# Performance work log

Hardware: AMD Instinct MI355X
Metric: run time of the kernel (lower is better)

The kernel has to match this reference:

```python
import jax, jax.numpy as jnp
import numpy as np

N, E, IN_C, HID_C, OUT_C = 50000, 800000, 64, 64, 8
NEG_SLOPE = 0.2


def setup_inputs() -> dict:
    key = jax.random.key(0)
    ks = jax.random.split(key, 12)
    return {
        "x": jax.random.normal(ks[0], (N, IN_C), dtype=jnp.float32),
        "edge_index": jax.random.randint(ks[1], (2, E), 0, N, dtype=jnp.int64),
        "edge_value": jax.random.uniform(ks[2], (E,), dtype=jnp.float32),
        "W1": jax.random.normal(ks[3], (IN_C, HID_C), dtype=jnp.float32) * 0.1,
        "a1_src": jax.random.normal(ks[4], (HID_C,), dtype=jnp.float32) * 0.1,
        "a1_dst": jax.random.normal(ks[5], (HID_C,), dtype=jnp.float32) * 0.1,
        "b1": jnp.zeros((HID_C,), dtype=jnp.float32),
        "W2": jax.random.normal(ks[6], (HID_C, OUT_C), dtype=jnp.float32) * 0.1,
        "a2_src": jax.random.normal(ks[7], (OUT_C,), dtype=jnp.float32) * 0.1,
        "a2_dst": jax.random.normal(ks[8], (OUT_C,), dtype=jnp.float32) * 0.1,
        "b2": jnp.zeros((OUT_C,), dtype=jnp.float32),
    }


def _rgat_conv(x, src, dst, edge_value, W, a_src, a_dst, b, n_nodes):
    # Linear transform: [N, out_c]
    h = x @ W
    # Per-node attention halves, gathered per edge -> per-edge logit
    e_src = h @ a_src  # [N]
    e_dst = h @ a_dst  # [N]
    logits = jax.nn.leaky_relu(e_src[src] + e_dst[dst], negative_slope=NEG_SLOPE)  # [E]
    # Segment softmax over destination neighborhoods (numerically stable)
    m = jax.ops.segment_max(logits, dst, num_segments=n_nodes)  # [N]
    ex = jnp.exp(logits - m[dst])
    denom = jax.ops.segment_sum(ex, dst, num_segments=n_nodes)  # [N]
    alpha = ex / (denom[dst] + 1e-16)  # [E]
    # Edge-weighted messages, scatter-aggregate to destinations
    msg = (alpha * edge_value)[:, None] * h[src]  # [E, out_c]
    out = jax.ops.segment_sum(msg, dst, num_segments=n_nodes)  # [N, out_c]
    return out + b


def reference(x, edge_index, edge_value, W1, a1_src, a1_dst, b1, W2, a2_src, a2_dst, b2):
    src, dst = edge_index[0], edge_index[1]
    n = x.shape[0]
    hid = _rgat_conv(x, src, dst, edge_value, W1, a1_src, a1_dst, b1, n)
    hid = jax.nn.relu(hid)
    out = _rgat_conv(hid, src, dst, edge_value, W2, a2_src, a2_dst, b2, n)
    return jax.nn.log_softmax(out, axis=1)
```

## Files before the change

kernel.cpp:

```cpp
#include <hip/hip_runtime.h>
#include <hip/hip_fp16.h>
#include <math.h>


#define CHUNK 4096
#define NBKT  256
#define CAP   6144

typedef unsigned long long ull;
typedef float v2f __attribute__((ext_vector_type(2)));

struct PartSmem {
    int lhist[NBKT], lbase[NBKT], lcur[NBKT], gbase[NBKT];
    ull buf[CHUNK];
};
struct GemmSmem {
    float4 Wl[64 * 16];
    float  Xt[64 * 64];
};
union FusedSmem { PartSmem p; GemmSmem g; };


__global__ void __launch_bounds__(256) part_gemm_kernel(
    const int* __restrict__ src, const int* __restrict__ dst,
    const float* __restrict__ ev, int* __restrict__ bcnt,
    ull* __restrict__ ped, int E, int nchunks,
    const float* __restrict__ x, const float* __restrict__ W,
    const float* __restrict__ a_src, const float* __restrict__ a_dst,
    unsigned* __restrict__ h, float* __restrict__ es, float* __restrict__ ed,
    int N)
{
    __shared__ FusedSmem sm;
    const int t = threadIdx.x;

    if (blockIdx.x < nchunks) {
        int e0 = blockIdx.x * CHUNK;
        int cnt = min(CHUNK, E - e0);
        sm.p.lhist[t] = 0;
        __syncthreads();
        for (int i = t; i < cnt; i += 256)
            atomicAdd(&sm.p.lhist[dst[e0 + i] >> 8], 1);
        __syncthreads();
        int myc = sm.p.lhist[t];
        sm.p.lbase[t] = myc;
        __syncthreads();
        for (int o = 1; o < 256; o <<= 1) {
            int add = (t >= o) ? sm.p.lbase[t - o] : 0;
            __syncthreads();
            sm.p.lbase[t] += add;
            __syncthreads();
        }
        int excl = sm.p.lbase[t] - myc;
        sm.p.gbase[t] = myc ? atomicAdd(&bcnt[t], myc) : 0;
        __syncthreads();
        sm.p.lbase[t] = excl;
        sm.p.lcur[t] = excl;
        __syncthreads();
        for (int i = t; i < cnt; i += 256) {
            int e = e0 + i;
            int d = dst[e];
            int b = d >> 8;
            unsigned p = (unsigned)src[e] | ((unsigned)(d & 255) << 16)
                       | ((unsigned)b << 24);
            ull q = (ull)p | ((ull)__float_as_uint(ev[e]) << 32);
            int r = atomicAdd(&sm.p.lcur[b], 1);
            sm.p.buf[r] = q;
        }
        __syncthreads();
        for (int i = t; i < cnt; i += 256) {
            ull q = sm.p.buf[i];
            int b = (int)((q >> 24) & 255);
            ped[(size_t)b * CAP + sm.p.gbase[b] + i - sm.p.lbase[b]] = q;
        }
        return;
    }

    const int n0 = (blockIdx.x - nchunks) * 64;

    #pragma unroll
    for (int i = 0; i < 4; ++i)
        sm.g.Wl[t + i * 256] = ((const float4*)W)[t + i * 256];

    #pragma unroll
    for (int i = 0; i < 4; ++i) {
        int f   = t + i * 256;
        int row = f >> 4, kq = f & 15;
        int grow = n0 + row;
        float4 v = make_float4(0.f, 0.f, 0.f, 0.f);
        if (grow < N) v = ((const float4*)x)[(size_t)grow * 16 + kq];
        int rs = row ^ ((kq & 3) << 2);
        sm.g.Xt[(kq * 4 + 0) * 64 + rs] = v.x;
        sm.g.Xt[(kq * 4 + 1) * 64 + rs] = v.y;
        sm.g.Xt[(kq * 4 + 2) * 64 + rs] = v.z;
        sm.g.Xt[(kq * 4 + 3) * 64 + rs] = v.w;
    }

    const int tx = t & 15;
    const int ty = t >> 4;
    const float4 asv = ((const float4*)a_src)[tx];
    const float4 adv = ((const float4*)a_dst)[tx];
    __syncthreads();

    float4 acc0 = make_float4(0.f,0.f,0.f,0.f);
    float4 acc1 = make_float4(0.f,0.f,0.f,0.f);
    float4 acc2 = make_float4(0.f,0.f,0.f,0.f);
    float4 acc3 = make_float4(0.f,0.f,0.f,0.f);

    #pragma unroll 8
    for (int k = 0; k < 64; ++k) {
        int swz = (k >> 2) & 3;
        const float4 xr = *(const float4*)&sm.g.Xt[k * 64 + ((ty ^ swz) << 2)];
        const float4 wv = sm.g.Wl[k * 16 + tx];
        acc0.x += xr.x * wv.x; acc0.y += xr.x * wv.y;
        acc0.z += xr.x * wv.z; acc0.w += xr.x * wv.w;
        acc1.x += xr.y * wv.x; acc1.y += xr.y * wv.y;
        acc1.z += xr.y * wv.z; acc1.w += xr.y * wv.w;
        acc2.x += xr.z * wv.x; acc2.y += xr.z * wv.y;
        acc2.z += xr.z * wv.z; acc2.w += xr.z * wv.w;
        acc3.x += xr.w * wv.x; acc3.y += xr.w * wv.y;
        acc3.z += xr.w * wv.z; acc3.w += xr.w * wv.w;
    }

    float4 accs[4] = {acc0, acc1, acc2, acc3};
    #pragma unroll
    for (int r = 0; r < 4; ++r) {
        int grow = n0 + ty * 4 + r;
        float4 a = accs[r];
        if (grow < N) {
            int lo = __builtin_amdgcn_cvt_pk_fp8_f32(a.x, a.y, 0, false);
            int pk = __builtin_amdgcn_cvt_pk_fp8_f32(a.z, a.w, lo, true);
            h[(size_t)grow * 16 + tx] = (unsigned)pk;
        }
        float ps = a.x * asv.x + a.y * asv.y + a.z * asv.z + a.w * asv.w;
        float pd = a.x * adv.x + a.y * adv.y + a.z * adv.z + a.w * adv.w;
        #pragma unroll
        for (int o = 8; o > 0; o >>= 1) {
            ps += __shfl_xor(ps, o);
            pd += __shfl_xor(pd, o);
        }
        if (tx == 0 && grow < N) { es[grow] = ps; ed[grow] = pd; }
    }
}


__global__ void __launch_bounds__(1024) csr2_kernel(
    const ull* __restrict__ ped, const int* __restrict__ bcnt,
    int* __restrict__ off, int* __restrict__ deg,
    ull* __restrict__ csre, int N)
{
    __shared__ int cl[256], sc[256], cur[256];
    int b = blockIdx.x, t = threadIdx.x;
    const int cnt = min(bcnt[b], CAP);
    const size_t base = (size_t)b * CAP;
    if (t < 256) cl[t] = 0;
    __syncthreads();
    for (int i = t; i < cnt; i += 1024)
        atomicAdd(&cl[(int)((ped[base + i] >> 16) & 255)], 1);
    __syncthreads();
    int myc = (t < 256) ? cl[t] : 0;
    if (t < 256) sc[t] = myc;
    __syncthreads();
    for (int o = 1; o < 256; o <<= 1) {
        int add = (t >= o && t < 256) ? sc[t - o] : 0;
        __syncthreads();
        if (t < 256) sc[t] += add;
        __syncthreads();
    }
    if (t < 256) {
        int excl = sc[t] - myc;
        int node = b * 256 + t;
        if (node < N) { off[node] = (int)base + excl; deg[node] = myc; }
        cur[t] = excl;
    }
    __syncthreads();
    for (int i = t; i < cnt; i += 1024) {
        ull q = ped[base + i];
        int dloc = (int)((q >> 16) & 255);
        int pos = (int)base + atomicAdd(&cur[dloc], 1);
        csre[pos] = (q & 0xFFFFFFFF00000000ull) | (q & 0xFFFFull);
    }
}


__global__ void __launch_bounds__(256) agg64_fused_kernel(
    const int* __restrict__ off, const int* __restrict__ deg,
    const ull* __restrict__ csre,
    const float* __restrict__ es, const float* __restrict__ ed,
    const unsigned* __restrict__ h, const float* __restrict__ b1,
    const float* __restrict__ W2, const float* __restrict__ a2s,
    const float* __restrict__ a2d, float* __restrict__ h2,
    float* __restrict__ es2, float* __restrict__ ed2, int N)
{
    __shared__ float W2s[64 * 8];
    const int t = threadIdx.x;
    if (t < 128) ((float4*)W2s)[t] = ((const float4*)W2)[t];

    const int wid = t >> 6, lane = t & 63;
    const int grp = lane >> 2;
    const int sl  = lane & 3;
    const int gbase = grp << 2;
    const int n = (blockIdx.x * 4 + wid) * 16 + grp;
    __syncthreads();
    if (n >= N) return;

    const int   beg = off[n];
    const int   dg  = deg[n];
    const float edn = ed[n];

    const float4 b1v0 = *(const float4*)&b1[sl * 16];
    const float4 b1v1 = *(const float4*)&b1[sl * 16 + 4];
    const float4 b1v2 = *(const float4*)&b1[sl * 16 + 8];
    const float4 b1v3 = *(const float4*)&b1[sl * 16 + 12];

    float acc[16];
    #pragma unroll
    for (int k = 0; k < 16; ++k) acc[k] = 0.f;
    float den = 0.f;

    for (int j0 = 0; j0 < dg; j0 += 4) {
        const int jj  = j0 + sl;
        const ull rec = csre[beg + min(jj, dg - 1)];
        const int sv  = (int)(rec & 0xFFFFull);
        const float evv = __uint_as_float((unsigned)(rec >> 32));
        float z = es[sv] + edn;
        float l = z > 0.f ? z : 0.2f * z;
        float q = (jj < dg) ? __expf(l) : 0.f;
        den += q;
        const float w = q * evv;
        #pragma unroll
        for (int ts = 0; ts < 4; ++ts) {
            const int   svt = __shfl(sv, gbase + ts);
            const float wt  = __shfl(w,  gbase + ts);
            const uint4 u = *(const uint4*)&h[(size_t)svt * 16 + sl * 4];
            v2f fa = __builtin_amdgcn_cvt_pk_f32_fp8((int)u.x, false);
            v2f fb = __builtin_amdgcn_cvt_pk_f32_fp8((int)u.x, true);
            v2f fc = __builtin_amdgcn_cvt_pk_f32_fp8((int)u.y, false);
            v2f fd = __builtin_amdgcn_cvt_pk_f32_fp8((int)u.y, true);
            v2f fe = __builtin_amdgcn_cvt_pk_f32_fp8((int)u.z, false);
            v2f ff = __builtin_amdgcn_cvt_pk_f32_fp8((int)u.z, true);
            v2f fg = __builtin_amdgcn_cvt_pk_f32_fp8((int)u.w, false);
            v2f fh = __builtin_amdgcn_cvt_pk_f32_fp8((int)u.w, true);
            acc[0]  += wt * fa.x; acc[1]  += wt * fa.y;
            acc[2]  += wt * fb.x; acc[3]  += wt * fb.y;
            acc[4]  += wt * fc.x; acc[5]  += wt * fc.y;
            acc[6]  += wt * fd.x; acc[7]  += wt * fd.y;
            acc[8]  += wt * fe.x; acc[9]  += wt * fe.y;
            acc[10] += wt * ff.x; acc[11] += wt * ff.y;
            acc[12] += wt * fg.x; acc[13] += wt * fg.y;
            acc[14] += wt * fh.x; acc[15] += wt * fh.y;
        }
    }

    den += __shfl_xor(den, 1);
    den += __shfl_xor(den, 2);
    const float inv = 1.f / (den + 1e-16f);

    float hid[16];
    hid[0]  = fmaxf(acc[0]  * inv + b1v0.x, 0.f);
    hid[1]  = fmaxf(acc[1]  * inv + b1v0.y, 0.f);
    hid[2]  = fmaxf(acc[2]  * inv + b1v0.z, 0.f);
    hid[3]  = fmaxf(acc[3]  * inv + b1v0.w, 0.f);
    hid[4]  = fmaxf(acc[4]  * inv + b1v1.x, 0.f);
    hid[5]  = fmaxf(acc[5]  * inv + b1v1.y, 0.f);
    hid[6]  = fmaxf(acc[6]  * inv + b1v1.z, 0.f);
    hid[7]  = fmaxf(acc[7]  * inv + b1v1.w, 0.f);
    hid[8]  = fmaxf(acc[8]  * inv + b1v2.x, 0.f);
    hid[9]  = fmaxf(acc[9]  * inv + b1v2.y, 0.f);
    hid[10] = fmaxf(acc[10] * inv + b1v2.z, 0.f);
    hid[11] = fmaxf(acc[11] * inv + b1v2.w, 0.f);
    hid[12] = fmaxf(acc[12] * inv + b1v3.x, 0.f);
    hid[13] = fmaxf(acc[13] * inv + b1v3.y, 0.f);
    hid[14] = fmaxf(acc[14] * inv + b1v3.z, 0.f);
    hid[15] = fmaxf(acc[15] * inv + b1v3.w, 0.f);

    float p[8];
    #pragma unroll
    for (int o = 0; o < 8; ++o) p[o] = 0.f;
    #pragma unroll
    for (int k = 0; k < 16; ++k) {
        const float4 wA = *(const float4*)&W2s[(sl * 16 + k) * 8];
        const float4 wB = *(const float4*)&W2s[(sl * 16 + k) * 8 + 4];
        p[0] += hid[k] * wA.x; p[1] += hid[k] * wA.y;
        p[2] += hid[k] * wA.z; p[3] += hid[k] * wA.w;
        p[4] += hid[k] * wB.x; p[5] += hid[k] * wB.y;
        p[6] += hid[k] * wB.z; p[7] += hid[k] * wB.w;
    }
    float s4[4];
    {
        const bool hi = (sl & 1);
        #pragma unroll
        for (int k = 0; k < 4; ++k) {
            float keep = hi ? p[k + 4] : p[k];
            float send = hi ? p[k]     : p[k + 4];
            s4[k] = keep + __shfl_xor(send, 1);
        }
    }
    float s2[2];
    {
        const bool hi = (sl & 2);
        #pragma unroll
        for (int k = 0; k < 2; ++k) {
            float keep = hi ? s4[k + 2] : s4[k];
            float send = hi ? s4[k]     : s4[k + 2];
            s2[k] = keep + __shfl_xor(send, 2);
        }
    }
    const int oo = 4 * (sl & 1) + 2 * ((sl >> 1) & 1);

    float tsv = s2[0] * a2s[oo] + s2[1] * a2s[oo + 1];
    float tdv = s2[0] * a2d[oo] + s2[1] * a2d[oo + 1];
    tsv += __shfl_xor(tsv, 1); tdv += __shfl_xor(tdv, 1);
    tsv += __shfl_xor(tsv, 2); tdv += __shfl_xor(tdv, 2);

    *(float2*)&h2[(size_t)n * 8 + oo] = make_float2(s2[0], s2[1]);
    if (sl == 0) { es2[n] = tsv; ed2[n] = tdv; }
}


__global__ void __launch_bounds__(256) agg8_lsm_kernel(
    const int* __restrict__ off, const int* __restrict__ deg,
    const ull* __restrict__ csre,
    const float* __restrict__ es, const float* __restrict__ ed,
    const float* __restrict__ h2, const float* __restrict__ b,
    float* __restrict__ out, int N)
{
    const int t = threadIdx.x;
    const int wid = t >> 6, lane = t & 63;
    const int grp = lane >> 2;
    const int sl  = lane & 3;
    const int gbase = grp << 2;
    const int n = (blockIdx.x * 4 + wid) * 16 + grp;
    if (n >= N) return;

    const int   beg = off[n];
    const int   dg  = deg[n];
    const float edn = ed[n];
    const float bc0 = b[2 * sl], bc1 = b[2 * sl + 1];

    float a0 = 0.f, a1 = 0.f, den = 0.f;

    for (int j0 = 0; j0 < dg; j0 += 4) {
        const int jj  = j0 + sl;
        const ull rec = csre[beg + min(jj, dg - 1)];
        const int sv  = (int)(rec & 0xFFFFull);
        const float evv = __uint_as_float((unsigned)(rec >> 32));
        float z = es[sv] + edn;
        float l = z > 0.f ? z : 0.2f * z;
        float q = (jj < dg) ? __expf(l) : 0.f;
        den += q;
        const float w = q * evv;
        #pragma unroll
        for (int ts = 0; ts < 4; ++ts) {
            const int   svt = __shfl(sv, gbase + ts);
            const float wt  = __shfl(w,  gbase + ts);
            const float2 f = *(const float2*)&h2[(size_t)svt * 8 + 2 * sl];
            a0 += wt * f.x;
            a1 += wt * f.y;
        }
    }

    den += __shfl_xor(den, 1);
    den += __shfl_xor(den, 2);
    const float inv = 1.f / (den + 1e-16f);
    float v0 = a0 * inv + bc0;
    float v1 = a1 * inv + bc1;

    float vm = fmaxf(v0, v1);
    vm = fmaxf(vm, __shfl_xor(vm, 1));
    vm = fmaxf(vm, __shfl_xor(vm, 2));
    float s = __expf(v0 - vm) + __expf(v1 - vm);
    s += __shfl_xor(s, 1);
    s += __shfl_xor(s, 2);
    float lse = vm + logf(s);
    *(float2*)&out[(size_t)n * 8 + 2 * sl] = make_float2(v0 - lse, v1 - lse);
}


extern "C" void kernel_launch(void* const* d_in, const int* in_sizes, int n_in,
                              void* d_out, int out_size, void* d_ws, size_t ws_size,
                              hipStream_t stream)
{
    const float* x   = (const float*)d_in[0];
    const int*   ei  = (const int*)d_in[1];
    const float* ev  = (const float*)d_in[2];
    const float* W1  = (const float*)d_in[3];
    const float* a1s = (const float*)d_in[4];
    const float* a1d = (const float*)d_in[5];
    const float* b1  = (const float*)d_in[6];
    const float* W2  = (const float*)d_in[7];
    const float* a2s = (const float*)d_in[8];
    const float* a2d = (const float*)d_in[9];
    const float* b2  = (const float*)d_in[10];
    float* out = (float*)d_out;

    const int N = in_sizes[0] / 64;
    const int E = in_sizes[2];
    const int* srcp = ei;
    const int* dstp = ei + E;
    const int nchunks = (E + CHUNK - 1) / CHUNK;
    const int ngemm   = (N + 63) / 64;
    const int nbuck = (N + 255) / 256;

    ull*   ped  = (ull*)d_ws;
    ull*   csre = ped + (size_t)NBKT * CAP;
    int*   bcnt = (int*)(csre + (size_t)NBKT * CAP);
    int*   off  = bcnt + NBKT;
    int*   deg  = off + N;
    float* es1  = (float*)(deg + N);
    float* ed1  = es1 + N;
    float* es2  = ed1 + N;
    float* ed2  = es2 + N;
    unsigned* h1 = (unsigned*)(ed2 + N);
    float* h2   = (float*)(h1 + (size_t)N * 16);

    hipMemsetAsync(bcnt, 0, NBKT * sizeof(int), stream);

    part_gemm_kernel<<<nchunks + ngemm, 256, 0, stream>>>(
        srcp, dstp, ev, bcnt, ped, E, nchunks,
        x, W1, a1s, a1d, h1, es1, ed1, N);

    csr2_kernel<<<nbuck, 1024, 0, stream>>>(ped, bcnt, off, deg, csre, N);

    agg64_fused_kernel<<<(N + 63) / 64, 256, 0, stream>>>(
        off, deg, csre, es1, ed1, h1, b1, W2, a2s, a2d, h2, es2, ed2, N);

    agg8_lsm_kernel<<<(N + 63) / 64, 256, 0, stream>>>(
        off, deg, csre, es2, ed2, h2, b2, out, N);
}
```

Baseline: 140.4 us.

## Merge four kernels into one cooperative persistent kernel with grid syncs

Replaces the partition/GEMM, CSR build, layer-1 aggregation and layer-2 aggregation launches with one cooperative kernel. Blocks stride over the work items of each phase and meet at grid.sync() barriers between phases. The goal is to remove per-launch overhead and the gaps between kernels. In exchange, occupancy is capped to the co-resident grid, the CSR phase now runs with 256 threads per bucket instead of 1024, and grid-wide barriers cost time of their own.

Measured after the change: 356.7 us. +154.1%, slower.

```diff
diff --git a/kernel.cpp b/kernel.cpp
--- a/kernel.cpp
+++ b/kernel.cpp
@@ -1,6 +1,8 @@
 #include <hip/hip_runtime.h>
-#include <hip/hip_fp16.h>
+#include <hip/hip_cooperative_groups.h>
 #include <math.h>
+
+namespace cg = cooperative_groups;
 
 
 #define CHUNK 4096
@@ -20,26 +22,148 @@
 };
 union FusedSmem { PartSmem p; GemmSmem g; };
 
-
-__global__ void __launch_bounds__(256) part_gemm_kernel(
+__global__ void __launch_bounds__(256, 4) mega_kernel(
     const int* __restrict__ src, const int* __restrict__ dst,
     const float* __restrict__ ev, int* __restrict__ bcnt,
     ull* __restrict__ ped, int E, int nchunks,
-    const float* __restrict__ x, const float* __restrict__ W,
-    const float* __restrict__ a_src, const float* __restrict__ a_dst,
-    unsigned* __restrict__ h, float* __restrict__ es, float* __restrict__ ed,
-    int N)
+    const float* __restrict__ x, const float* __restrict__ W1,
+    const float* __restrict__ a1s, const float* __restrict__ a1d,
+    unsigned* __restrict__ h1, float* __restrict__ es1, float* __restrict__ ed1,
+    int* __restrict__ off, int* __restrict__ deg, ull* __restrict__ csre,
+    const float* __restrict__ b1, const float* __restrict__ W2,
+    const float* __restrict__ a2s, const float* __restrict__ a2d,
+    float* __restrict__ h2, float* __restrict__ es2, float* __restrict__ ed2,
+    const float* __restrict__ b2, float* __restrict__ out, int N)
 {
+    cg::grid_group grid = cg::this_grid();
     __shared__ FusedSmem sm;
-    const int t = threadIdx.x;
-
-    if (blockIdx.x < nchunks) {
-        int e0 = blockIdx.x * CHUNK;
-        int cnt = min(CHUNK, E - e0);
+    __shared__ float W2s[64 * 8];
+
+    const int t  = threadIdx.x;
+    const int nb = gridDim.x;
+    const int ngemm = (N + 63) / 64;
+    const int nbuck = (N + 255) / 256;
+    const int nt    = (N + 63) / 64;
+
+    for (int w = blockIdx.x; w < nchunks + ngemm; w += nb) {
+        if (w < nchunks) {
+            int e0 = w * CHUNK;
+            int cnt = min(CHUNK, E - e0);
+            sm.p.lhist[t] = 0;
+            __syncthreads();
+            for (int i = t; i < cnt; i += 256)
+                atomicAdd(&sm.p.lhist[dst[e0 + i] >> 8], 1);
+            __syncthreads();
+            int myc = sm.p.lhist[t];
+            sm.p.lbase[t] = myc;
+            __syncthreads();
+            for (int o = 1; o < 256; o <<= 1) {
+                int add = (t >= o) ? sm.p.lbase[t - o] : 0;
+                __syncthreads();
+                sm.p.lbase[t] += add;
+                __syncthreads();
+            }
+            int excl = sm.p.lbase[t] - myc;
+            sm.p.gbase[t] = myc ? atomicAdd(&bcnt[t], myc) : 0;
+            __syncthreads();
+            sm.p.lbase[t] = excl;
+            sm.p.lcur[t] = excl;
+            __syncthreads();
+            for (int i = t; i < cnt; i += 256) {
+                int e = e0 + i;
+                int d = dst[e];
+                int b = d >> 8;
+                unsigned p = (unsigned)src[e] | ((unsigned)(d & 255) << 16)
+                           | ((unsigned)b << 24);
+                ull q = (ull)p | ((ull)__float_as_uint(ev[e]) << 32);
+                int r = atomicAdd(&sm.p.lcur[b], 1);
+                sm.p.buf[r] = q;
+            }
+            __syncthreads();
+            for (int i = t; i < cnt; i += 256) {
+                ull q = sm.p.buf[i];
+                int b = (int)((q >> 24) & 255);
+                ped[(size_t)b * CAP + sm.p.gbase[b] + i - sm.p.lbase[b]] = q;
+            }
+        } else {
+            const int n0 = (w - nchunks) * 64;
+
+            #pragma unroll
+            for (int i = 0; i < 4; ++i)
+                sm.g.Wl[t + i * 256] = ((const float4*)W1)[t + i * 256];
+
+            #pragma unroll
+            for (int i = 0; i < 4; ++i) {
+                int f   = t + i * 256;
+                int row = f >> 4, kq = f & 15;
+                int grow = n0 + row;
+                float4 v = make_float4(0.f, 0.f, 0.f, 0.f);
+                if (grow < N) v = ((const float4*)x)[(size_t)grow * 16 + kq];
+                int rs = row ^ ((kq & 3) << 2);
+                sm.g.Xt[(kq * 4 + 0) * 64 + rs] = v.x;
+                sm.g.Xt[(kq * 4 + 1) * 64 + rs] = v.y;
+                sm.g.Xt[(kq * 4 + 2) * 64 + rs] = v.z;
+                sm.g.Xt[(kq * 4 + 3) * 64 + rs] = v.w;
+            }
+
+            const int tx = t & 15;
+            const int ty = t >> 4;
+            const float4 asv = ((const float4*)a1s)[tx];
+            const float4 adv = ((const float4*)a1d)[tx];
+            __syncthreads();
+
+            float4 acc0 = make_float4(0.f,0.f,0.f,0.f);
+            float4 acc1 = make_float4(0.f,0.f,0.f,0.f);
+            float4 acc2 = make_float4(0.f,0.f,0.f,0.f);
+            float4 acc3 = make_float4(0.f,0.f,0.f,0.f);
+
+            #pragma unroll 8
+            for (int k = 0; k < 64; ++k) {
+                int swz = (k >> 2) & 3;
+                const float4 xr = *(const float4*)&sm.g.Xt[k * 64 + ((ty ^ swz) << 2)];
+                const float4 wv = sm.g.Wl[k * 16 + tx];
+                acc0.x += xr.x * wv.x; acc0.y += xr.x * wv.y;
+                acc0.z += xr.x * wv.z; acc0.w += xr.x * wv.w;
+                acc1.x += xr.y * wv.x; acc1.y += xr.y * wv.y;
+                acc1.z += xr.y * wv.z; acc1.w += xr.y * wv.w;
+                acc2.x += xr.z * wv.x; acc2.y += xr.z * wv.y;
+                acc2.z += xr.z * wv.z; acc2.w += xr.z * wv.w;
+                acc3.x += xr.w * wv.x; acc3.y += xr.w * wv.y;
+                acc3.z += xr.w * wv.z; acc3.w += xr.w * wv.w;
+            }
+
+            float4 accs[4] = {acc0, acc1, acc2, acc3};
+            #pragma unroll
+            for (int r = 0; r < 4; ++r) {
+                int grow = n0 + ty * 4 + r;
+                float4 a = accs[r];
+                if (grow < N) {
+                    int lo = __builtin_amdgcn_cvt_pk_fp8_f32(a.x, a.y, 0, false);
+                    int pk = __builtin_amdgcn_cvt_pk_fp8_f32(a.z, a.w, lo, true);
+                    h1[(size_t)grow * 16 + tx] = (unsigned)pk;
+                }
+                float ps = a.x * asv.x + a.y * asv.y + a.z * asv.z + a.w * asv.w;
+                float pd = a.x * adv.x + a.y * adv.y + a.z * adv.z + a.w * adv.w;
+                #pragma unroll
+                for (int o = 8; o > 0; o >>= 1) {
+                    ps += __shfl_xor(ps, o);
+                    pd += __shfl_xor(pd, o);
+                }
+                if (tx == 0 && grow < N) { es1[grow] = ps; ed1[grow] = pd; }
+            }
+        }
+        __syncthreads();
+    }
+
+    grid.sync();
+
+    for (int b = blockIdx.x; b < nbuck; b += nb) {
+        const int cnt = min(bcnt[b], CAP);
+        const size_t base = (size_t)b * CAP;
         sm.p.lhist[t] = 0;
         __syncthreads();
         for (int i = t; i < cnt; i += 256)
-            atomicAdd(&sm.p.lhist[dst[e0 + i] >> 8], 1);
+            atomicAdd(&sm.p.lhist[(int)((ped[base + i] >> 16) & 255)], 1);
         __syncthreads();
         int myc = sm.p.lhist[t];
         sm.p.lbase[t] = myc;
@@ -51,328 +175,192 @@
             __syncthreads();
         }
         int excl = sm.p.lbase[t] - myc;
-        sm.p.gbase[t] = myc ? atomicAdd(&bcnt[t], myc) : 0;
-        __syncthreads();
-        sm.p.lbase[t] = excl;
-        sm.p.lcur[t] = excl;
-        __syncthreads();
-        for (int i = t; i < cnt; i += 256) {
-            int e = e0 + i;
-            int d = dst[e];
-            int b = d >> 8;
-            unsigned p = (unsigned)src[e] | ((unsigned)(d & 255) << 16)
-                       | ((unsigned)b << 24);
-            ull q = (ull)p | ((ull)__float_as_uint(ev[e]) << 32);
-            int r = atomicAdd(&sm.p.lcur[b], 1);
-            sm.p.buf[r] = q;
-        }
-        __syncthreads();
-        for (int i = t; i < cnt; i += 256) {
-            ull q = sm.p.buf[i];
-            int b = (int)((q >> 24) & 255);
-            ped[(size_t)b * CAP + sm.p.gbase[b] + i - sm.p.lbase[b]] = q;
-        }
-        return;
-    }
-
-    const int n0 = (blockIdx.x - nchunks) * 64;
-
-    #pragma unroll
-    for (int i = 0; i < 4; ++i)
-        sm.g.Wl[t + i * 256] = ((const float4*)W)[t + i * 256];
-
-    #pragma unroll
-    for (int i = 0; i < 4; ++i) {
-        int f   = t + i * 256;
-        int row = f >> 4, kq = f & 15;
-        int grow = n0 + row;
-        float4 v = make_float4(0.f, 0.f, 0.f, 0.f);
-        if (grow < N) v = ((const float4*)x)[(size_t)grow * 16 + kq];
-        int rs = row ^ ((kq & 3) << 2);
-        sm.g.Xt[(kq * 4 + 0) * 64 + rs] = v.x;
-        sm.g.Xt[(kq * 4 + 1) * 64 + rs] = v.y;
-        sm.g.Xt[(kq * 4 + 2) * 64 + rs] = v.z;
-        sm.g.Xt[(kq * 4 + 3) * 64 + rs] = v.w;
-    }
-
-    const int tx = t & 15;
-    const int ty = t >> 4;
-    const float4 asv = ((const float4*)a_src)[tx];
-    const float4 adv = ((const float4*)a_dst)[tx];
-    __syncthreads();
-
-    float4 acc0 = make_float4(0.f,0.f,0.f,0.f);
-    float4 acc1 = make_float4(0.f,0.f,0.f,0.f);
-    float4 acc2 = make_float4(0.f,0.f,0.f,0.f);
-    float4 acc3 = make_float4(0.f,0.f,0.f,0.f);
-
-    #pragma unroll 8
-    for (int k = 0; k < 64; ++k) {
-        int swz = (k >> 2) & 3;
-        const float4 xr = *(const float4*)&sm.g.Xt[k * 64 + ((ty ^ swz) << 2)];
-        const float4 wv = sm.g.Wl[k * 16 + tx];
-        acc0.x += xr.x * wv.x; acc0.y += xr.x * wv.y;
-        acc0.z += xr.x * wv.z; acc0.w += xr.x * wv.w;
-        acc1.x += xr.y * wv.x; acc1.y += xr.y * wv.y;
-        acc1.z += xr.y * wv.z; acc1.w += xr.y * wv.w;
-        acc2.x += xr.z * wv.x; acc2.y += xr.z * wv.y;
-        acc2.z += xr.z * wv.z; acc2.w += xr.z * wv.w;
-        acc3.x += xr.w * wv.x; acc3.y += xr.w * wv.y;
-        acc3.z += xr.w * wv.z; acc3.w += xr.w * wv.w;
-    }
-
-    float4 accs[4] = {acc0, acc1, acc2, acc3};
-    #pragma unroll
-    for (int r = 0; r < 4; ++r) {
-        int grow = n0 + ty * 4 + r;
-        float4 a = accs[r];
-        if (grow < N) {
-            int lo = __builtin_amdgcn_cvt_pk_fp8_f32(a.x, a.y, 0, false);
-            int pk = __builtin_amdgcn_cvt_pk_fp8_f32(a.z, a.w, lo, true);
-            h[(size_t)grow * 16 + tx] = (unsigned)pk;
-        }
-        float ps = a.x * asv.x + a.y * asv.y + a.z * asv.z + a.w * asv.w;
-        float pd = a.x * adv.x + a.y * adv.y + a.z * adv.z + a.w * adv.w;
-        #pragma unroll
-        for (int o = 8; o > 0; o >>= 1) {
-            ps += __shfl_xor(ps, o);
-            pd += __shfl_xor(pd, o);
-        }
-        if (tx == 0 && grow < N) { es[grow] = ps; ed[grow] = pd; }
-    }
-}
-
-
-__global__ void __launch_bounds__(1024) csr2_kernel(
-    const ull* __restrict__ ped, const int* __restrict__ bcnt,
-    int* __restrict__ off, int* __restrict__ deg,
-    ull* __restrict__ csre, int N)
-{
-    __shared__ int cl[256], sc[256], cur[256];
-    int b = blockIdx.x, t = threadIdx.x;
-    const int cnt = min(bcnt[b], CAP);
-    const size_t base = (size_t)b * CAP;
-    if (t < 256) cl[t] = 0;
-    __syncthreads();
-    for (int i = t; i < cnt; i += 1024)
-        atomicAdd(&cl[(int)((ped[base + i] >> 16) & 255)], 1);
-    __syncthreads();
-    int myc = (t < 256) ? cl[t] : 0;
-    if (t < 256) sc[t] = myc;
-    __syncthreads();
-    for (int o = 1; o < 256; o <<= 1) {
-        int add = (t >= o && t < 256) ? sc[t - o] : 0;
-        __syncthreads();
-        if (t < 256) sc[t] += add;
-        __syncthreads();
-    }
-    if (t < 256) {
-        int excl = sc[t] - myc;
         int node = b * 256 + t;
         if (node < N) { off[node] = (int)base + excl; deg[node] = myc; }
-        cur[t] = excl;
+        sm.p.lcur[t] = excl;
+        __syncthreads();
+        for (int i = t; i < cnt; i += 256) {
+            ull q = ped[base + i];
+            int dloc = (int)((q >> 16) & 255);
+            int pos = (int)base + atomicAdd(&sm.p.lcur[dloc], 1);
+            csre[pos] = (q & 0xFFFFFFFF00000000ull) | (q & 0xFFFFull);
+        }
+        __syncthreads();
     }
+
+    grid.sync();
+
+    if (t < 128) ((float4*)W2s)[t] = ((const float4*)W2)[t];
     __syncthreads();
-    for (int i = t; i < cnt; i += 1024) {
-        ull q = ped[base + i];
-        int dloc = (int)((q >> 16) & 255);
-        int pos = (int)base + atomicAdd(&cur[dloc], 1);
-        csre[pos] = (q & 0xFFFFFFFF00000000ull) | (q & 0xFFFFull);
-    }
-}
-
-
-__global__ void __launch_bounds__(256) agg64_fused_kernel(
-    const int* __restrict__ off, const int* __restrict__ deg,
-    const ull* __restrict__ csre,
-    const float* __restrict__ es, const float* __restrict__ ed,
-    const unsigned* __restrict__ h, const float* __restrict__ b1,
-    const float* __restrict__ W2, const float* __restrict__ a2s,
-    const float* __restrict__ a2d, float* __restrict__ h2,
-    float* __restrict__ es2, float* __restrict__ ed2, int N)
-{
-    __shared__ float W2s[64 * 8];
-    const int t = threadIdx.x;
-    if (t < 128) ((float4*)W2s)[t] = ((const float4*)W2)[t];
 
     const int wid = t >> 6, lane = t & 63;
-    const int grp = lane >> 2;
-    const int sl  = lane & 3;
-    const int gbase = grp << 2;
-    const int n = (blockIdx.x * 4 + wid) * 16 + grp;
-    __syncthreads();
-    if (n >= N) return;
-
-    const int   beg = off[n];
-    const int   dg  = deg[n];
-    const float edn = ed[n];
-
-    const float4 b1v0 = *(const float4*)&b1[sl * 16];
-    const float4 b1v1 = *(const float4*)&b1[sl * 16 + 4];
-    const float4 b1v2 = *(const float4*)&b1[sl * 16 + 8];
-    const float4 b1v3 = *(const float4*)&b1[sl * 16 + 12];
-
-    float acc[16];
-    #pragma unroll
-    for (int k = 0; k < 16; ++k) acc[k] = 0.f;
-    float den = 0.f;
-
-    for (int j0 = 0; j0 < dg; j0 += 4) {
-        const int jj  = j0 + sl;
-        const ull rec = csre[beg + min(jj, dg - 1)];
-        const int sv  = (int)(rec & 0xFFFFull);
-        const float evv = __uint_as_float((unsigned)(rec >> 32));
-        float z = es[sv] + edn;
-        float l = z > 0.f ? z : 0.2f * z;
-        float q = (jj < dg) ? __expf(l) : 0.f;
-        den += q;
-        const float w = q * evv;
-        #pragma unroll
-        for (int ts = 0; ts < 4; ++ts) {
-            const int   svt = __shfl(sv, gbase + ts);
-            const float wt  = __shfl(w,  gbase + ts);
-            const uint4 u = *(const uint4*)&h[(size_t)svt * 16 + sl * 4];
-            v2f fa = __builtin_amdgcn_cvt_pk_f32_fp8((int)u.x, false);
-            v2f fb = __builtin_amdgcn_cvt_pk_f32_fp8((int)u.x, true);
-            v2f fc = __builtin_amdgcn_cvt_pk_f32_fp8((int)u.y, false);
-            v2f fd = __builtin_amdgcn_cvt_pk_f32_fp8((int)u.y, true);
-            v2f fe = __builtin_amdgcn_cvt_pk_f32_fp8((int)u.z, false);
-            v2f ff = __builtin_amdgcn_cvt_pk_f32_fp8((int)u.z, true);
-            v2f fg = __builtin_amdgcn_cvt_pk_f32_fp8((int)u.w, false);
-            v2f fh = __builtin_amdgcn_cvt_pk_f32_fp8((int)u.w, true);
-            acc[0]  += wt * fa.x; acc[1]  += wt * fa.y;
-            acc[2]  += wt * fb.x; acc[3]  += wt * fb.y;
-            acc[4]  += wt * fc.x; acc[5]  += wt * fc.y;
-            acc[6]  += wt * fd.x; acc[7]  += wt * fd.y;
-            acc[8]  += wt * fe.x; acc[9]  += wt * fe.y;
-            acc[10] += wt * ff.x; acc[11] += wt * ff.y;
-            acc[12] += wt * fg.x; acc[13] += wt * fg.y;
-            acc[14] += wt * fh.x; acc[15] += wt * fh.y;
+    const int grp = lane >> 2, sl = lane & 3, gbase = grp << 2;
+
+    for (int tile = blockIdx.x; tile < nt; tile += nb) {
+        const int n = (tile * 4 + wid) * 16 + grp;
+        if (n < N) {
+            const int   beg = off[n];
+            const int   dg  = deg[n];
+            const float edn = ed1[n];
+
+            const float4 b1v0 = *(const float4*)&b1[sl * 16];
+            const float4 b1v1 = *(const float4*)&b1[sl * 16 + 4];
+            const float4 b1v2 = *(const float4*)&b1[sl * 16 + 8];
+            const float4 b1v3 = *(const float4*)&b1[sl * 16 + 12];
+
+            float acc[16];
+            #pragma unroll
+            for (int k = 0; k < 16; ++k) acc[k] = 0.f;
+            float den = 0.f;
+
+            for (int j0 = 0; j0 < dg; j0 += 4) {
+                const int jj  = j0 + sl;
+                const ull rec = csre[beg + min(jj, dg - 1)];
+                const int sv  = (int)(rec & 0xFFFFull);
+                const float evv = __uint_as_float((unsigned)(rec >> 32));
+                float z = es1[sv] + edn;
+                float l = z > 0.f ? z : 0.2f * z;
+                float q = (jj < dg) ? __expf(l) : 0.f;
+                den += q;
+                const float w = q * evv;
+                #pragma unroll
+                for (int ts = 0; ts < 4; ++ts) {
+                    const int   svt = __shfl(sv, gbase + ts);
+                    const float wt  = __shfl(w,  gbase + ts);
+                    const uint4 u = *(const uint4*)&h1[(size_t)svt * 16 + sl * 4];
+                    v2f fa = __builtin_amdgcn_cvt_pk_f32_fp8((int)u.x, false);
+                    v2f fb = __builtin_amdgcn_cvt_pk_f32_fp8((int)u.x, true);
+                    v2f fc = __builtin_amdgcn_cvt_pk_f32_fp8((int)u.y, false);
+                    v2f fd = __builtin_amdgcn_cvt_pk_f32_fp8((int)u.y, true);
+                    v2f fe = __builtin_amdgcn_cvt_pk_f32_fp8((int)u.z, false);
+                    v2f ff = __builtin_amdgcn_cvt_pk_f32_fp8((int)u.z, true);
+                    v2f fg = __builtin_amdgcn_cvt_pk_f32_fp8((int)u.w, false);
+                    v2f fh = __builtin_amdgcn_cvt_pk_f32_fp8((int)u.w, true);
+                    acc[0]  += wt * fa.x; acc[1]  += wt * fa.y;
+                    acc[2]  += wt * fb.x; acc[3]  += wt * fb.y;
+                    acc[4]  += wt * fc.x; acc[5]  += wt * fc.y;
+                    acc[6]  += wt * fd.x; acc[7]  += wt * fd.y;
+                    acc[8]  += wt * fe.x; acc[9]  += wt * fe.y;
+                    acc[10] += wt * ff.x; acc[11] += wt * ff.y;
+                    acc[12] += wt * fg.x; acc[13] += wt * fg.y;
+                    acc[14] += wt * fh.x; acc[15] += wt * fh.y;
+                }
+            }
+
+            den += __shfl_xor(den, 1);
+            den += __shfl_xor(den, 2);
+            const float inv = 1.f / (den + 1e-16f);
+
+            float hid[16];
+            hid[0]  = fmaxf(acc[0]  * inv + b1v0.x, 0.f);
+            hid[1]  = fmaxf(acc[1]  * inv + b1v0.y, 0.f);
+            hid[2]  = fmaxf(acc[2]  * inv + b1v0.z, 0.f);
+            hid[3]  = fmaxf(acc[3]  * inv + b1v0.w, 0.f);
+            hid[4]  = fmaxf(acc[4]  * inv + b1v1.x, 0.f);
+            hid[5]  = fmaxf(acc[5]  * inv + b1v1.y, 0.f);
+            hid[6]  = fmaxf(acc[6]  * inv + b1v1.z, 0.f);
+            hid[7]  = fmaxf(acc[7]  * inv + b1v1.w, 0.f);
+            hid[8]  = fmaxf(acc[8]  * inv + b1v2.x, 0.f);
+            hid[9]  = fmaxf(acc[9]  * inv + b1v2.y, 0.f);
+            hid[10] = fmaxf(acc[10] * inv + b1v2.z, 0.f);
+            hid[11] = fmaxf(acc[11] * inv + b1v2.w, 0.f);
+            hid[12] = fmaxf(acc[12] * inv + b1v3.x, 0.f);
+            hid[13] = fmaxf(acc[13] * inv + b1v3.y, 0.f);
+            hid[14] = fmaxf(acc[14] * inv + b1v3.z, 0.f);
+            hid[15] = fmaxf(acc[15] * inv + b1v3.w, 0.f);
+
+            float p[8];
+            #pragma unroll
+            for (int o = 0; o < 8; ++o) p[o] = 0.f;
+            #pragma unroll
+            for (int k = 0; k < 16; ++k) {
+                const float4 wA = *(const float4*)&W2s[(sl * 16 + k) * 8];
+                const float4 wB = *(const float4*)&W2s[(sl * 16 + k) * 8 + 4];
+                p[0] += hid[k] * wA.x; p[1] += hid[k] * wA.y;
+                p[2] += hid[k] * wA.z; p[3] += hid[k] * wA.w;
+                p[4] += hid[k] * wB.x; p[5] += hid[k] * wB.y;
+                p[6] += hid[k] * wB.z; p[7] += hid[k] * wB.w;
+            }
+            float s4[4];
+            {
+                const bool hi = (sl & 1);
+                #pragma unroll
+                for (int k = 0; k < 4; ++k) {
+                    float keep = hi ? p[k + 4] : p[k];
+                    float send = hi ? p[k]     : p[k + 4];
+                    s4[k] = keep + __shfl_xor(send, 1);
+                }
+            }
+            float s2[2];
+            {
+                const bool hi = (sl & 2);
+                #pragma unroll
+                for (int k = 0; k < 2; ++k) {
+                    float keep = hi ? s4[k + 2] : s4[k];
+                    float send = hi ? s4[k]     : s4[k + 2];
+                    s2[k] = keep + __shfl_xor(send, 2);
+                }
+            }
+            const int oo = 4 * (sl & 1) + 2 * ((sl >> 1) & 1);
+
+            float tsv = s2[0] * a2s[oo] + s2[1] * a2s[oo + 1];
+            float tdv = s2[0] * a2d[oo] + s2[1] * a2d[oo + 1];
+            tsv += __shfl_xor(tsv, 1); tdv += __shfl_xor(tdv, 1);
+            tsv += __shfl_xor(tsv, 2); tdv += __shfl_xor(tdv, 2);
+
+            *(float2*)&h2[(size_t)n * 8 + oo] = make_float2(s2[0], s2[1]);
+            if (sl == 0) { es2[n] = tsv; ed2[n] = tdv; }
         }
     }
 
-    den += __shfl_xor(den, 1);
-    den += __shfl_xor(den, 2);
-    const float inv = 1.f / (den + 1e-16f);
-
-    float hid[16];
-    hid[0]  = fmaxf(acc[0]  * inv + b1v0.x, 0.f);
-    hid[1]  = fmaxf(acc[1]  * inv + b1v0.y, 0.f);
-    hid[2]  = fmaxf(acc[2]  * inv + b1v0.z, 0.f);
-    hid[3]  = fmaxf(acc[3]  * inv + b1v0.w, 0.f);
-    hid[4]  = fmaxf(acc[4]  * inv + b1v1.x, 0.f);
-    hid[5]  = fmaxf(acc[5]  * inv + b1v1.y, 0.f);
-    hid[6]  = fmaxf(acc[6]  * inv + b1v1.z, 0.f);
-    hid[7]  = fmaxf(acc[7]  * inv + b1v1.w, 0.f);
-    hid[8]  = fmaxf(acc[8]  * inv + b1v2.x, 0.f);
-    hid[9]  = fmaxf(acc[9]  * inv + b1v2.y, 0.f);
-    hid[10] = fmaxf(acc[10] * inv + b1v2.z, 0.f);
-    hid[11] = fmaxf(acc[11] * inv + b1v2.w, 0.f);
-    hid[12] = fmaxf(acc[12] * inv + b1v3.x, 0.f);
-    hid[13] = fmaxf(acc[13] * inv + b1v3.y, 0.f);
-    hid[14] = fmaxf(acc[14] * inv + b1v3.z, 0.f);
-    hid[15] = fmaxf(acc[15] * inv + b1v3.w, 0.f);
-
-    float p[8];
-    #pragma unroll
-    for (int o = 0; o < 8; ++o) p[o] = 0.f;
-    #pragma unroll
-    for (int k = 0; k < 16; ++k) {
-        const float4 wA = *(const float4*)&W2s[(sl * 16 + k) * 8];
-        const float4 wB = *(const float4*)&W2s[(sl * 16 + k) * 8 + 4];
-        p[0] += hid[k] * wA.x; p[1] += hid[k] * wA.y;
-        p[2] += hid[k] * wA.z; p[3] += hid[k] * wA.w;
-        p[4] += hid[k] * wB.x; p[5] += hid[k] * wB.y;
-        p[6] += hid[k] * wB.z; p[7] += hid[k] * wB.w;
-    }
-    float s4[4];
-    {
-        const bool hi = (sl & 1);
-        #pragma unroll
-        for (int k = 0; k < 4; ++k) {
-            float keep = hi ? p[k + 4] : p[k];
-            float send = hi ? p[k]     : p[k + 4];
-            s4[k] = keep + __shfl_xor(send, 1);
+    grid.sync();
+
+    for (int tile = blockIdx.x; tile < nt; tile += nb) {
+        const int n = (tile * 4 + wid) * 16 + grp;
+        if (n < N) {
+            const int   beg = off[n];
+            const int   dg  = deg[n];
+            const float edn = ed2[n];
+            const float bc0 = b2[2 * sl], bc1 = b2[2 * sl + 1];
+
+            float a0 = 0.f, a1 = 0.f, den = 0.f;
+
+            for (int j0 = 0; j0 < dg; j0 += 4) {
+                const int jj  = j0 + sl;
+                const ull rec = csre[beg + min(jj, dg - 1)];
+                const int sv  = (int)(rec & 0xFFFFull);
+                const float evv = __uint_as_float((unsigned)(rec >> 32));
+                float z = es2[sv] + edn;
+                float l = z > 0.f ? z : 0.2f * z;
+                float q = (jj < dg) ? __expf(l) : 0.f;
+                den += q;
+                const float w = q * evv;
+                #pragma unroll
+                for (int ts = 0; ts < 4; ++ts) {
+                    const int   svt = __shfl(sv, gbase + ts);
+                    const float wt  = __shfl(w,  gbase + ts);
+                    const float2 f = *(const float2*)&h2[(size_t)svt * 8 + 2 * sl];
+                    a0 += wt * f.x;
+                    a1 += wt * f.y;
+                }
+            }
+
+            den += __shfl_xor(den, 1);
+            den += __shfl_xor(den, 2);
+            const float inv = 1.f / (den + 1e-16f);
+            float v0 = a0 * inv + bc0;
+            float v1 = a1 * inv + bc1;
+
+            float vm = fmaxf(v0, v1);
+            vm = fmaxf(vm, __shfl_xor(vm, 1));
+            vm = fmaxf(vm, __shfl_xor(vm, 2));
+            float s = __expf(v0 - vm) + __expf(v1 - vm);
+            s += __shfl_xor(s, 1);
+            s += __shfl_xor(s, 2);
+            float lse = vm + logf(s);
+            *(float2*)&out[(size_t)n * 8 + 2 * sl] = make_float2(v0 - lse, v1 - lse);
         }
     }
-    float s2[2];
-    {
-        const bool hi = (sl & 2);
-        #pragma unroll
-        for (int k = 0; k < 2; ++k) {
-            float keep = hi ? s4[k + 2] : s4[k];
-            float send = hi ? s4[k]     : s4[k + 2];
-            s2[k] = keep + __shfl_xor(send, 2);
-        }
-    }
-    const int oo = 4 * (sl & 1) + 2 * ((sl >> 1) & 1);
-
-    float tsv = s2[0] * a2s[oo] + s2[1] * a2s[oo + 1];
-    float tdv = s2[0] * a2d[oo] + s2[1] * a2d[oo + 1];
-    tsv += __shfl_xor(tsv, 1); tdv += __shfl_xor(tdv, 1);
-    tsv += __shfl_xor(tsv, 2); tdv += __shfl_xor(tdv, 2);
-
-    *(float2*)&h2[(size_t)n * 8 + oo] = make_float2(s2[0], s2[1]);
-    if (sl == 0) { es2[n] = tsv; ed2[n] = tdv; }
-}
-
-
-__global__ void __launch_bounds__(256) agg8_lsm_kernel(
-    const int* __restrict__ off, const int* __restrict__ deg,
-    const ull* __restrict__ csre,
-    const float* __restrict__ es, const float* __restrict__ ed,
-    const float* __restrict__ h2, const float* __restrict__ b,
-    float* __restrict__ out, int N)
-{
-    const int t = threadIdx.x;
-    const int wid = t >> 6, lane = t & 63;
-    const int grp = lane >> 2;
-    const int sl  = lane & 3;
-    const int gbase = grp << 2;
-    const int n = (blockIdx.x * 4 + wid) * 16 + grp;
-    if (n >= N) return;
-
-    const int   beg = off[n];
-    const int   dg  = deg[n];
-    const float edn = ed[n];
-    const float bc0 = b[2 * sl], bc1 = b[2 * sl + 1];
-
-    float a0 = 0.f, a1 = 0.f, den = 0.f;
-
-    for (int j0 = 0; j0 < dg; j0 += 4) {
-        const int jj  = j0 + sl;
-        const ull rec = csre[beg + min(jj, dg - 1)];
-        const int sv  = (int)(rec & 0xFFFFull);
-        const float evv = __uint_as_float((unsigned)(rec >> 32));
-        float z = es[sv] + edn;
-        float l = z > 0.f ? z : 0.2f * z;
-        float q = (jj < dg) ? __expf(l) : 0.f;
-        den += q;
-        const float w = q * evv;
-        #pragma unroll
-        for (int ts = 0; ts < 4; ++ts) {
-            const int   svt = __shfl(sv, gbase + ts);
-            const float wt  = __shfl(w,  gbase + ts);
-            const float2 f = *(const float2*)&h2[(size_t)svt * 8 + 2 * sl];
-            a0 += wt * f.x;
-            a1 += wt * f.y;
-        }
-    }
-
-    den += __shfl_xor(den, 1);
-    den += __shfl_xor(den, 2);
-    const float inv = 1.f / (den + 1e-16f);
-    float v0 = a0 * inv + bc0;
-    float v1 = a1 * inv + bc1;
-
-    float vm = fmaxf(v0, v1);
-    vm = fmaxf(vm, __shfl_xor(vm, 1));
-    vm = fmaxf(vm, __shfl_xor(vm, 2));
-    float s = __expf(v0 - vm) + __expf(v1 - vm);
-    s += __shfl_xor(s, 1);
-    s += __shfl_xor(s, 2);
-    float lse = vm + logf(s);
-    *(float2*)&out[(size_t)n * 8 + 2 * sl] = make_float2(v0 - lse, v1 - lse);
 }
 
 
@@ -399,7 +387,6 @@
     const int* dstp = ei + E;
     const int nchunks = (E + CHUNK - 1) / CHUNK;
     const int ngemm   = (N + 63) / 64;
-    const int nbuck = (N + 255) / 256;
 
     ull*   ped  = (ull*)d_ws;
     ull*   csre = ped + (size_t)NBKT * CAP;
@@ -415,15 +402,24 @@
 
     hipMemsetAsync(bcnt, 0, NBKT * sizeof(int), stream);
 
-    part_gemm_kernel<<<nchunks + ngemm, 256, 0, stream>>>(
-        srcp, dstp, ev, bcnt, ped, E, nchunks,
-        x, W1, a1s, a1d, h1, es1, ed1, N);
-
-    csr2_kernel<<<nbuck, 1024, 0, stream>>>(ped, bcnt, off, deg, csre, N);
-
-    agg64_fused_kernel<<<(N + 63) / 64, 256, 0, stream>>>(
-        off, deg, csre, es1, ed1, h1, b1, W2, a2s, a2d, h2, es2, ed2, N);
-
-    agg8_lsm_kernel<<<(N + 63) / 64, 256, 0, stream>>>(
-        off, deg, csre, es2, ed2, h2, b2, out, N);
+    int maxb = 0;
+    if (hipOccupancyMaxActiveBlocksPerMultiprocessor(&maxb, mega_kernel, 256, 0)
+            != hipSuccess || maxb < 1)
+        maxb = 2;
+    int grid = maxb * 256;
+    const int work0 = nchunks + ngemm;
+    if (grid > work0) grid = work0;
+
+    void* args[] = {
+        (void*)&srcp, (void*)&dstp, (void*)&ev, (void*)&bcnt, (void*)&ped,
+        (void*)&E, (void*)&nchunks,
+        (void*)&x, (void*)&W1, (void*)&a1s, (void*)&a1d,
+        (void*)&h1, (void*)&es1, (void*)&ed1,
+        (void*)&off, (void*)&deg, (void*)&csre,
+        (void*)&b1, (void*)&W2, (void*)&a2s, (void*)&a2d,
+        (void*)&h2, (void*)&es2, (void*)&ed2,
+        (void*)&b2, (void*)&out, (void*)&N
+    };
+    hipLaunchCooperativeKernel((void*)mega_kernel, dim3(grid), dim3(256),
+                               args, 0, stream);
 }
```
